# Kernel optimization log

Measured on AMD Instinct MI355X. Metric: run time of the kernel, lower is better.

The kernel has to match this reference:

```python
import jax, jax.numpy as jnp
import numpy as np

B, N, D, C = 256, 2000, 512, 100


def setup_inputs() -> dict:
    key = jax.random.key(0)
    k1, k2, k3, k4 = jax.random.split(key, 4)
    inputs = jax.random.normal(k1, (B, D), dtype=jnp.float32)
    support_tensors = jax.random.normal(k2, (N, D), dtype=jnp.float32)
    label_idx = jax.random.randint(k3, (N,), 0, C)
    support_labels = jax.nn.one_hot(label_idx, C, dtype=jnp.float32)
    kernel_w = jax.random.normal(k4, (D,), dtype=jnp.float32) * 0.05
    kernel_b = jnp.zeros((), dtype=jnp.float32)
    return {
        "inputs": inputs,
        "support_tensors": support_tensors,
        "support_labels": support_labels,
        "kernel_w": kernel_w,
        "kernel_b": kernel_b,
    }


def reference(inputs, support_tensors, support_labels, kernel_w, kernel_b):
    # Pairwise Cartesian product (batch x support): |a - b|, shape [B, N, D]
    diff = jnp.abs(inputs[:, None, :] - support_tensors[None, :, :])
    # Siamese kernel: sigmoid(Dense(1)(|a-b|)) -> scores [B, N]
    pair_wise_scores = jax.nn.sigmoid(jnp.einsum("bnd,d->bn", diff, kernel_w) + kernel_b)
    # Per-class aggregation: matmul with one-hot labels, then mean per class
    class_sums = pair_wise_scores @ support_labels  # [B, C]
    class_counts = jnp.sum(support_labels, axis=0)  # [C]
    # tf.math.divide_no_nan semantics
    return jnp.where(class_counts != 0, class_sums / class_counts, 0.0)
```

## Files before the change

### kernel.cpp

```cpp
#include <hip/hip_runtime.h>

#define B_SZ 256
#define N_SZ 2000
#define N_PAD 2048
#define D_SZ 512
#define C_SZ 100
#define BT 4
#define JW 4
#define ZSPLIT 16
#define D4 (D_SZ / 4)
#define DC8 (D_SZ / 8)

typedef __fp16 h2 __attribute__((ext_vector_type(2)));

struct alignas(16) H8 { h2 x, y, z, w; };
struct alignas(8)  H4 { h2 lo, hi; };

static __device__ __forceinline__ h2 habs2(h2 v) {
    unsigned u = __builtin_bit_cast(unsigned, v) & 0x7FFF7FFFu;
    return __builtin_bit_cast(h2, u);
}

#if __has_builtin(__builtin_amdgcn_fdot2)
static __device__ __forceinline__ float DOT2(h2 d, h2 wv, float c) {
    return __builtin_amdgcn_fdot2(d, wv, c, false);
}
#else
static __device__ __forceinline__ float DOT2(h2 d, h2 wv, float c) {
    return c + (float)d.x * (float)wv.x + (float)d.y * (float)wv.y;
}
#endif

__global__ void setup_kernel(const float* __restrict__ labels,
                             const float* __restrict__ inputs,
                             const float* __restrict__ w,
                             const float4* __restrict__ sup4,
                             int* __restrict__ idx,
                             H4* __restrict__ inpH4,
                             H4* __restrict__ wH4,
                             H8* __restrict__ supH) {
    int bid = blockIdx.x, tid = threadIdx.x;
    if (bid < 512) {
        int t   = bid * 256 + tid;
        int n   = t >> 6;
        int dc8 = t & 63;
        H8 o = {};
        if (n < N_SZ) {
            float4 p = sup4[(size_t)n * D4 + 2 * dc8];
            float4 q = sup4[(size_t)n * D4 + 2 * dc8 + 1];
            o.x = __builtin_amdgcn_cvt_pkrtz(p.x, p.y);
            o.y = __builtin_amdgcn_cvt_pkrtz(p.z, p.w);
            o.z = __builtin_amdgcn_cvt_pkrtz(q.x, q.y);
            o.w = __builtin_amdgcn_cvt_pkrtz(q.z, q.w);
        }
        supH[(size_t)dc8 * N_PAD + n] = o;
    } else if (bid < 640) {
        int i4 = (bid - 512) * 256 + tid;
        float4 v = ((const float4*)inputs)[i4];
        H4 o;
        o.lo = __builtin_amdgcn_cvt_pkrtz(v.x, v.y);
        o.hi = __builtin_amdgcn_cvt_pkrtz(v.z, v.w);
        inpH4[i4] = o;
    } else if (bid < 648) {
        int n = (bid - 640) * 256 + tid;
        if (n < N_SZ) {
            const float4* row = (const float4*)(labels + (size_t)n * C_SZ);
            int c = 0;
#pragma unroll
            for (int j = 0; j < C_SZ / 4; ++j) {
                float4 v = row[j];
                if (v.x > 0.5f) c = 4 * j + 0;
                if (v.y > 0.5f) c = 4 * j + 1;
                if (v.z > 0.5f) c = 4 * j + 2;
                if (v.w > 0.5f) c = 4 * j + 3;
            }
            idx[n] = c;
        }
    } else {
        if (tid < D_SZ / 4) {
            float4 v = ((const float4*)w)[tid];
            H4 o;
            o.lo = __builtin_amdgcn_cvt_pkrtz(v.x, v.y);
            o.hi = __builtin_amdgcn_cvt_pkrtz(v.z, v.w);
            wH4[tid] = o;
        }
    }
}

__global__ __launch_bounds__(256, 3) void score_kernel(
    const H8* __restrict__ inpH8,
    const H8* __restrict__ supH,
    const H8* __restrict__ wH8,
    __fp16* __restrict__ S16)
{
    int tid = threadIdx.x;
    int b0  = blockIdx.x * BT;
    int dc0 = blockIdx.y * JW;

    unsigned vz = 0;
    asm volatile("" : "+v"(vz));

    H8 af[BT][JW];
    H8 wf[JW];
#pragma unroll
    for (int i = 0; i < BT; ++i) {
        const H8* ap = inpH8 + (size_t)(b0 + i) * DC8 + dc0 + vz;
#pragma unroll
        for (int j = 0; j < JW; ++j) af[i][j] = ap[j];
    }
    {
        const H8* wp = wH8 + dc0 + vz;
#pragma unroll
        for (int j = 0; j < JW; ++j) wf[j] = wp[j];
    }

    const H8* sp0 = supH + (size_t)(dc0 + 0) * N_PAD + tid;
    const H8* sp1 = supH + (size_t)(dc0 + 1) * N_PAD + tid;
    const H8* sp2 = supH + (size_t)(dc0 + 2) * N_PAD + tid;
    const H8* sp3 = supH + (size_t)(dc0 + 3) * N_PAD + tid;

    __fp16* Sp0 = S16 + ((size_t)blockIdx.y * B_SZ + b0) * N_PAD + tid;

#define STEP(J, SV)                                                  \
    {                                                                \
        H8 wv = wf[J];                                               \
        _Pragma("unroll") for (int i = 0; i < BT; ++i) {             \
            H8 a = af[i][J];                                         \
            acc[i] = DOT2(habs2(a.x - SV.x), wv.x, acc[i]);          \
            acc[i] = DOT2(habs2(a.y - SV.y), wv.y, acc[i]);          \
            acc[i] = DOT2(habs2(a.z - SV.z), wv.z, acc[i]);          \
            acc[i] = DOT2(habs2(a.w - SV.w), wv.w, acc[i]);          \
        }                                                            \
    }

    H8 sv0 = sp0[0], sv1 = sp1[0], sv2 = sp2[0], sv3 = sp3[0];

#pragma unroll 1
    for (int n0 = 0; n0 < N_PAD - 256; n0 += 256) {
        float acc[BT] = {0.f, 0.f, 0.f, 0.f};
        H8 nx0 = sp0[n0 + 256];
        STEP(0, sv0);
        H8 nx1 = sp1[n0 + 256];
        STEP(1, sv1);
        H8 nx2 = sp2[n0 + 256];
        STEP(2, sv2);
        H8 nx3 = sp3[n0 + 256];
        STEP(3, sv3);
#pragma unroll
        for (int i = 0; i < BT; ++i)
            Sp0[(size_t)i * N_PAD + n0] = (__fp16)acc[i];
        sv0 = nx0; sv1 = nx1; sv2 = nx2; sv3 = nx3;
    }
    {
        float acc[BT] = {0.f, 0.f, 0.f, 0.f};
        STEP(0, sv0); STEP(1, sv1); STEP(2, sv2); STEP(3, sv3);
#pragma unroll
        for (int i = 0; i < BT; ++i)
            Sp0[(size_t)i * N_PAD + (N_PAD - 256)] = (__fp16)acc[i];
    }
#undef STEP
}

__global__ void agg_kernel(const __fp16* __restrict__ S16,
                           const int* __restrict__ idx,
                           const float* __restrict__ bias_p,
                           float* __restrict__ out) {
    __shared__ float sums[C_SZ];
    __shared__ float cnts[C_SZ];
    int b = blockIdx.x;
    int t = threadIdx.x;
    if (t < C_SZ) { sums[t] = 0.f; cnts[t] = 0.f; }
    __syncthreads();
    float bias = *bias_p;
    for (int n = t; n < N_SZ; n += 1024) {
        float logit = bias;
#pragma unroll
        for (int z = 0; z < ZSPLIT; ++z)
            logit += (float)S16[((size_t)z * B_SZ + b) * N_PAD + n];
        float s = 1.0f / (1.0f + __expf(-logit));
        int c = idx[n];
        atomicAdd(&sums[c], s);
        atomicAdd(&cnts[c], 1.0f);
    }
    __syncthreads();
    if (t < C_SZ) {
        float cnt = cnts[t];
        out[(size_t)b * C_SZ + t] = (cnt != 0.f) ? sums[t] / cnt : 0.f;
    }
}

extern "C" void kernel_launch(void* const* d_in, const int* in_sizes, int n_in,
                              void* d_out, int out_size, void* d_ws, size_t ws_size,
                              hipStream_t stream) {
    const float* inputs  = (const float*)d_in[0];
    const float* support = (const float*)d_in[1];
    const float* labels  = (const float*)d_in[2];
    const float* w       = (const float*)d_in[3];
    const float* bias    = (const float*)d_in[4];
    float* out = (float*)d_out;

    int*     idx  = (int*)d_ws;
    H4*      wH4  = (H4*)((char*)d_ws + 8192);
    H4*      inpH = (H4*)((char*)d_ws + 16384);
    H8*      supH = (H8*)((char*)d_ws + 524288);
    __fp16*  S16  = (__fp16*)((char*)d_ws + 4 * 1024 * 1024);

    setup_kernel<<<dim3(649), dim3(256), 0, stream>>>(
        labels, inputs, w, (const float4*)support, idx, inpH, wH4, supH);

    dim3 grid(B_SZ / BT, ZSPLIT);
    score_kernel<<<grid, dim3(256), 0, stream>>>(
        (const H8*)inpH, supH, (const H8*)wH4, S16);

    agg_kernel<<<dim3(B_SZ), dim3(1024), 0, stream>>>(S16, idx, bias, out);
}
```

Before: 39.42 us.

## Pack four batch partial scores into one 8-byte store and raise occupancy

The score kernel now packs its four per-row fp16 partial sums into a single uint2 store per thread instead of four scattered 2-byte stores, which changes the intermediate layout to [z][b/4][n][4]. The aggregation kernel reads the 8-byte element and extracts its own half, which wastes some read bandwidth because each block loads data belonging to three other rows. Launch bounds go from 3 to 4 waves per SIMD, and empty asm barriers pin the input and weight fragments in registers so the compiler does not rematerialise or spill them.

Result: slower. 42.44 us (+7.7%).

```diff
diff --git a/kernel.cpp b/kernel.cpp
--- a/kernel.cpp
+++ b/kernel.cpp
@@ -10,6 +10,7 @@
 #define ZSPLIT 16
 #define D4 (D_SZ / 4)
 #define DC8 (D_SZ / 8)
+#define NB4 (B_SZ / BT)
 
 typedef __fp16 h2 __attribute__((ext_vector_type(2)));
 
@@ -87,14 +88,15 @@
     }
 }
 
-__global__ __launch_bounds__(256, 3) void score_kernel(
+__global__ __launch_bounds__(256, 4) void score_kernel(
     const H8* __restrict__ inpH8,
     const H8* __restrict__ supH,
     const H8* __restrict__ wH8,
-    __fp16* __restrict__ S16)
+    uint2* __restrict__ S16p)
 {
     int tid = threadIdx.x;
-    int b0  = blockIdx.x * BT;
+    int b4  = blockIdx.x;
+    int b0  = b4 * BT;
     int dc0 = blockIdx.y * JW;
 
     unsigned vz = 0;
@@ -113,13 +115,24 @@
 #pragma unroll
         for (int j = 0; j < JW; ++j) wf[j] = wp[j];
     }
+
+#pragma unroll
+    for (int i = 0; i < BT; ++i)
+#pragma unroll
+        for (int j = 0; j < JW; ++j)
+            asm volatile("" : "+v"(af[i][j].x), "+v"(af[i][j].y),
+                              "+v"(af[i][j].z), "+v"(af[i][j].w));
+#pragma unroll
+    for (int j = 0; j < JW; ++j)
+        asm volatile("" : "+v"(wf[j].x), "+v"(wf[j].y),
+                          "+v"(wf[j].z), "+v"(wf[j].w));
 
     const H8* sp0 = supH + (size_t)(dc0 + 0) * N_PAD + tid;
     const H8* sp1 = supH + (size_t)(dc0 + 1) * N_PAD + tid;
     const H8* sp2 = supH + (size_t)(dc0 + 2) * N_PAD + tid;
     const H8* sp3 = supH + (size_t)(dc0 + 3) * N_PAD + tid;
 
-    __fp16* Sp0 = S16 + ((size_t)blockIdx.y * B_SZ + b0) * N_PAD + tid;
+    uint2* Sp0 = S16p + ((size_t)blockIdx.y * NB4 + b4) * N_PAD + tid;
 
 #define STEP(J, SV)                                                  \
     {                                                                \
@@ -131,6 +144,16 @@
             acc[i] = DOT2(habs2(a.z - SV.z), wv.z, acc[i]);          \
             acc[i] = DOT2(habs2(a.w - SV.w), wv.w, acc[i]);          \
         }                                                            \
+    }
+
+#define PACK_STORE(N0)                                               \
+    {                                                                \
+        h2 lo = __builtin_amdgcn_cvt_pkrtz(acc[0], acc[1]);          \
+        h2 hi = __builtin_amdgcn_cvt_pkrtz(acc[2], acc[3]);          \
+        uint2 u;                                                     \
+        u.x = __builtin_bit_cast(unsigned, lo);                      \
+        u.y = __builtin_bit_cast(unsigned, hi);                      \
+        Sp0[N0] = u;                                                 \
     }
 
     H8 sv0 = sp0[0], sv1 = sp1[0], sv2 = sp2[0], sv3 = sp3[0];
@@ -146,22 +169,19 @@
         STEP(2, sv2);
         H8 nx3 = sp3[n0 + 256];
         STEP(3, sv3);
-#pragma unroll
-        for (int i = 0; i < BT; ++i)
-            Sp0[(size_t)i * N_PAD + n0] = (__fp16)acc[i];
+        PACK_STORE(n0);
         sv0 = nx0; sv1 = nx1; sv2 = nx2; sv3 = nx3;
     }
     {
         float acc[BT] = {0.f, 0.f, 0.f, 0.f};
         STEP(0, sv0); STEP(1, sv1); STEP(2, sv2); STEP(3, sv3);
-#pragma unroll
-        for (int i = 0; i < BT; ++i)
-            Sp0[(size_t)i * N_PAD + (N_PAD - 256)] = (__fp16)acc[i];
+        PACK_STORE(N_PAD - 256);
     }
 #undef STEP
-}
-
-__global__ void agg_kernel(const __fp16* __restrict__ S16,
+#undef PACK_STORE
+}
+
+__global__ void agg_kernel(const uint2* __restrict__ S16p,
                            const int* __restrict__ idx,
                            const float* __restrict__ bias_p,
                            float* __restrict__ out) {
@@ -169,14 +189,21 @@
     __shared__ float cnts[C_SZ];
     int b = blockIdx.x;
     int t = threadIdx.x;
+    int b4 = b >> 2;
+    int q  = b & 3;
+    int sh = (q & 1) * 16;
     if (t < C_SZ) { sums[t] = 0.f; cnts[t] = 0.f; }
     __syncthreads();
     float bias = *bias_p;
     for (int n = t; n < N_SZ; n += 1024) {
         float logit = bias;
 #pragma unroll
-        for (int z = 0; z < ZSPLIT; ++z)
-            logit += (float)S16[((size_t)z * B_SZ + b) * N_PAD + n];
+        for (int z = 0; z < ZSPLIT; ++z) {
+            uint2 v = S16p[((size_t)z * NB4 + b4) * N_PAD + n];
+            unsigned half = (q & 2) ? v.y : v.x;
+            unsigned short bits = (unsigned short)(half >> sh);
+            logit += (float)__builtin_bit_cast(__fp16, bits);
+        }
         float s = 1.0f / (1.0f + __expf(-logit));
         int c = idx[n];
         atomicAdd(&sums[c], s);
@@ -199,18 +226,18 @@
     const float* bias    = (const float*)d_in[4];
     float* out = (float*)d_out;
 
-    int*     idx  = (int*)d_ws;
-    H4*      wH4  = (H4*)((char*)d_ws + 8192);
-    H4*      inpH = (H4*)((char*)d_ws + 16384);
-    H8*      supH = (H8*)((char*)d_ws + 524288);
-    __fp16*  S16  = (__fp16*)((char*)d_ws + 4 * 1024 * 1024);
+    int*    idx  = (int*)d_ws;
+    H4*     wH4  = (H4*)((char*)d_ws + 8192);
+    H4*     inpH = (H4*)((char*)d_ws + 16384);
+    H8*     supH = (H8*)((char*)d_ws + 524288);
+    uint2*  S16p = (uint2*)((char*)d_ws + 4 * 1024 * 1024);
 
     setup_kernel<<<dim3(649), dim3(256), 0, stream>>>(
         labels, inputs, w, (const float4*)support, idx, inpH, wH4, supH);
 
-    dim3 grid(B_SZ / BT, ZSPLIT);
+    dim3 grid(NB4, ZSPLIT);
     score_kernel<<<grid, dim3(256), 0, stream>>>(
-        (const H8*)inpH, supH, (const H8*)wH4, S16);
-
-    agg_kernel<<<dim3(B_SZ), dim3(1024), 0, stream>>>(S16, idx, bias, out);
-}
+        (const H8*)inpH, supH, (const H8*)wH4, S16p);
+
+    agg_kernel<<<dim3(B_SZ), dim3(1024), 0, stream>>>(S16p, idx, bias, out);
+}
```
